# Kernel tuning notes

Hardware: AMD Instinct MI355X
Metric: run time of the kernel (lower is better)

The kernel has to match this reference:

```python
import jax, jax.numpy as jnp
import numpy as np

T = 100.0  # temperature, from init_kwargs
B = 4096
D = 128
NUM_CLASSES = 10


def setup_inputs() -> dict:
    key = jax.random.key(0)
    kx, ky = jax.random.split(key)
    x = jax.random.normal(kx, (B, D), dtype=jnp.float32)
    y = jax.random.randint(ky, (B,), 0, NUM_CLASSES, dtype=jnp.int64)
    return {"x": x, "y": y}


def reference(x, y):
    # Pairwise squared Euclidean distances: dist[i,j] = ||x_i - x_j||^2
    sq = jnp.sum(x * x, axis=1)                      # [b]
    dist = sq[:, None] + sq[None, :] - 2.0 * (x @ x.T)  # [b, b]
    dist = jnp.maximum(dist, 0.0)                    # clamp fp error; diag -> 0

    e = jnp.exp(-dist / T)                           # [b, b]; e[i,i] = 1

    b = x.shape[0]
    same = (y[:, None] == y[None, :])                # same-label mask
    not_self = ~jnp.eye(b, dtype=bool)

    # numerator: sum over j != i with y[j] == y[i]
    num = jnp.sum(jnp.where(same & not_self, e, 0.0), axis=1)  # [b]
    # denominator: sum over ALL j, including j == i (exp(0) = 1), as in the
    # original loop where the denominator accumulates unconditionally
    den = jnp.sum(e, axis=1)                         # [b]

    return jnp.mean(-jnp.log(num / den))
```

## Files before the change

kernel.cpp:

```cpp
#include <hip/hip_runtime.h>
#include <hip/hip_bf16.h>

#define NB 4096
#define DD 128

typedef short v8s __attribute__((ext_vector_type(8)));
typedef float v4f __attribute__((ext_vector_type(4)));


__global__ __launch_bounds__(256) void prep_kernel(const float* __restrict__ x,
        float* __restrict__ sq, float* __restrict__ num, float* __restrict__ den,
        float* __restrict__ out, unsigned short* __restrict__ xb) {
    int tid = threadIdx.x;
    int row = blockIdx.x * 8 + (tid >> 5);
    int lane = tid & 31;
    const float4* xg = (const float4*)x;
    float4 v = xg[row * 32 + lane];
    __hip_bfloat16 h0 = __float2bfloat16(v.x), h1 = __float2bfloat16(v.y);
    __hip_bfloat16 h2 = __float2bfloat16(v.z), h3 = __float2bfloat16(v.w);
    ushort4 u4;
    u4.x = *(unsigned short*)&h0; u4.y = *(unsigned short*)&h1;
    u4.z = *(unsigned short*)&h2; u4.w = *(unsigned short*)&h3;
    ((ushort4*)xb)[row * 32 + lane] = u4;
    float s = v.x * v.x + v.y * v.y + v.z * v.z + v.w * v.w;
    #pragma unroll
    for (int off = 16; off > 0; off >>= 1) s += __shfl_down(s, off);
    if (lane == 0) sq[row] = s;
    int gid = blockIdx.x * 256 + tid;
    if (gid < NB) { num[gid] = 0.f; den[gid] = 0.f; }
    if (gid == 0) out[0] = 0.f;
}

__global__ __launch_bounds__(256) void snn_mfma(const unsigned short* __restrict__ xb,
        const int* __restrict__ y, const float* __restrict__ sqg,
        float* __restrict__ num, float* __restrict__ den) {
    __shared__ __align__(16) union {
        unsigned short tiles[2 * 128 * 136];
        float part[2 * 128 * 34];
    } sm;
    __shared__ float sqi[128], sqj[128];
    __shared__ int yi[128], yj[128];

    const int tid = threadIdx.x;
    const int wave = tid >> 6;
    const int lane = tid & 63;
    const int wm = wave >> 1;
    const int wn = wave & 1;
    const int lr = lane & 15;
    const int q  = lane >> 4;
    const int i0 = blockIdx.x * 128;
    const int j0 = blockIdx.y * 128;

    const v8s* xg = (const v8s*)xb;
    unsigned short* At = sm.tiles;
    unsigned short* Bt = sm.tiles + 128 * 136;

    #pragma unroll
    for (int r = 0; r < 8; ++r) {
        int c = r * 256 + tid;
        int row = c >> 4, cc = c & 15;
        *(v8s*)&At[row * 136 + cc * 8] = xg[(i0 + row) * 16 + cc];
        *(v8s*)&Bt[row * 136 + cc * 8] = xg[(j0 + row) * 16 + cc];
    }
    if (tid < 128) {
        sqi[tid] = sqg[i0 + tid]; sqj[tid] = sqg[j0 + tid];
        yi[tid] = y[i0 + tid];    yj[tid] = y[j0 + tid];
    }
    __syncthreads();

    v4f acc[4][4];
    #pragma unroll
    for (int mt = 0; mt < 4; ++mt)
        #pragma unroll
        for (int nt = 0; nt < 4; ++nt)
            #pragma unroll
            for (int r = 0; r < 4; ++r) acc[mt][nt][r] = 0.f;

    #pragma unroll
    for (int kk = 0; kk < 4; ++kk) {
        v8s af[4], bf[4];
        #pragma unroll
        for (int mt = 0; mt < 4; ++mt)
            af[mt] = *(const v8s*)&At[(wm * 64 + mt * 16 + lr) * 136 + kk * 32 + q * 8];
        #pragma unroll
        for (int nt = 0; nt < 4; ++nt)
            bf[nt] = *(const v8s*)&Bt[(wn * 64 + nt * 16 + lr) * 136 + kk * 32 + q * 8];
        #pragma unroll
        for (int mt = 0; mt < 4; ++mt)
            #pragma unroll
            for (int nt = 0; nt < 4; ++nt)
                acc[mt][nt] = __builtin_amdgcn_mfma_f32_16x16x32_bf16(
                    af[mt], bf[nt], acc[mt][nt], 0, 0, 0);
    }

    __syncthreads();

    float sqj_r[4]; int yj_r[4], jg[4];
    #pragma unroll
    for (int nt = 0; nt < 4; ++nt) {
        int jc = wn * 64 + nt * 16 + lr;
        sqj_r[nt] = sqj[jc]; yj_r[nt] = yj[jc]; jg[nt] = j0 + jc;
    }
    #pragma unroll
    for (int mt = 0; mt < 4; ++mt) {
        #pragma unroll
        for (int r = 0; r < 4; ++r) {
            int rloc = wm * 64 + mt * 16 + q * 4 + r;
            float si = sqi[rloc]; int yir = yi[rloc]; int ig = i0 + rloc;
            float n = 0.f, d = 0.f;
            #pragma unroll
            for (int nt = 0; nt < 4; ++nt) {
                float dist = fmaxf(si + sqj_r[nt] - 2.f * acc[mt][nt][r], 0.f);
                float e = __builtin_amdgcn_exp2f(dist * -0.014426950408889634f);
                d += e;
                bool ok = (yir == yj_r[nt]) && (ig != jg[nt]);
                n += ok ? e : 0.f;
            }
            *(float2*)&sm.part[((wn * 128 + rloc) * 17 + lr) * 2] = make_float2(n, d);
        }
    }
    __syncthreads();

    {
        int row = tid >> 1, h = tid & 1;
        const float2* p = (const float2*)&sm.part[(h * 128 + row) * 34];
        float sn = 0.f, sd = 0.f;
        #pragma unroll
        for (int c = 0; c < 16; ++c) { float2 v = p[c]; sn += v.x; sd += v.y; }
        sn += __shfl_down(sn, 1); sd += __shfl_down(sd, 1);
        if (h == 0) {
            atomicAdd(&num[i0 + row], sn);
            atomicAdd(&den[i0 + row], sd);
        }
    }
}

__global__ __launch_bounds__(256) void snn_final(const float* __restrict__ num,
        const float* __restrict__ den, float* __restrict__ out) {
    __shared__ float wsum[4];
    int i = blockIdx.x * 256 + threadIdx.x;
    float l = -__logf(num[i] / den[i]);
    #pragma unroll
    for (int off = 32; off > 0; off >>= 1) l += __shfl_down(l, off);
    int wid = threadIdx.x >> 6;
    if ((threadIdx.x & 63) == 0) wsum[wid] = l;
    __syncthreads();
    if (threadIdx.x == 0) {
        float s = wsum[0] + wsum[1] + wsum[2] + wsum[3];
        atomicAdd(out, s * (1.0f / NB));
    }
}

extern "C" void kernel_launch(void* const* d_in, const int* in_sizes, int n_in,
                              void* d_out, int out_size, void* d_ws, size_t ws_size,
                              hipStream_t stream) {
    const float* x = (const float*)d_in[0];
    const int*   y = (const int*)d_in[1];
    float* out = (float*)d_out;
    float* sq  = (float*)d_ws;
    float* num = sq + NB;
    float* den = num + NB;
    unsigned short* xb = (unsigned short*)(den + NB);

    prep_kernel<<<NB / 8, 256, 0, stream>>>(x, sq, num, den, out, xb);
    dim3 grid(NB / 128, NB / 128);
    snn_mfma<<<grid, 256, 0, stream>>>(xb, y, sq, num, den);
    snn_final<<<NB / 256, 256, 0, stream>>>(num, den, out);
}
```

Measured before the change: 71.20 us.

## Fuse bf16 conversion and norms into MFMA kernel; replace atomics with partials

Removes the separate prep kernel. The main MFMA kernel now loads fp32 x directly, converts each tile to bf16 in shared memory and computes the row squared norms from those bf16 tiles. Per-row num/den atomics are replaced by a per-column-block partials buffer, which the final kernel sums before taking logs. This saves a launch, the zeroing pass and atomic contention. In exchange each block reads twice as many bytes (fp32 instead of bf16) with redundant conversion work, and the norms are now computed from bf16-rounded values.

```diff
diff --git a/kernel.cpp b/kernel.cpp
--- a/kernel.cpp
+++ b/kernel.cpp
@@ -2,38 +2,18 @@
 #include <hip/hip_bf16.h>
 
 #define NB 4096
-#define DD 128
 
 typedef short v8s __attribute__((ext_vector_type(8)));
 typedef float v4f __attribute__((ext_vector_type(4)));
 
-
-__global__ __launch_bounds__(256) void prep_kernel(const float* __restrict__ x,
-        float* __restrict__ sq, float* __restrict__ num, float* __restrict__ den,
-        float* __restrict__ out, unsigned short* __restrict__ xb) {
-    int tid = threadIdx.x;
-    int row = blockIdx.x * 8 + (tid >> 5);
-    int lane = tid & 31;
-    const float4* xg = (const float4*)x;
-    float4 v = xg[row * 32 + lane];
-    __hip_bfloat16 h0 = __float2bfloat16(v.x), h1 = __float2bfloat16(v.y);
-    __hip_bfloat16 h2 = __float2bfloat16(v.z), h3 = __float2bfloat16(v.w);
-    ushort4 u4;
-    u4.x = *(unsigned short*)&h0; u4.y = *(unsigned short*)&h1;
-    u4.z = *(unsigned short*)&h2; u4.w = *(unsigned short*)&h3;
-    ((ushort4*)xb)[row * 32 + lane] = u4;
-    float s = v.x * v.x + v.y * v.y + v.z * v.z + v.w * v.w;
-    #pragma unroll
-    for (int off = 16; off > 0; off >>= 1) s += __shfl_down(s, off);
-    if (lane == 0) sq[row] = s;
-    int gid = blockIdx.x * 256 + tid;
-    if (gid < NB) { num[gid] = 0.f; den[gid] = 0.f; }
-    if (gid == 0) out[0] = 0.f;
+__device__ __forceinline__ float bf2f(unsigned short u) {
+    return __uint_as_float(((unsigned int)u) << 16);
 }
 
-__global__ __launch_bounds__(256) void snn_mfma(const unsigned short* __restrict__ xb,
-        const int* __restrict__ y, const float* __restrict__ sqg,
-        float* __restrict__ num, float* __restrict__ den) {
+
+__global__ __launch_bounds__(256) void snn_mfma(const float* __restrict__ x,
+        const int* __restrict__ y, float2* __restrict__ part,
+        float* __restrict__ out) {
     __shared__ __align__(16) union {
         unsigned short tiles[2 * 128 * 136];
         float part[2 * 128 * 34];
@@ -51,22 +31,52 @@
     const int i0 = blockIdx.x * 128;
     const int j0 = blockIdx.y * 128;
 
-    const v8s* xg = (const v8s*)xb;
+    if (blockIdx.x == 0 && blockIdx.y == 0 && tid == 0) out[0] = 0.f;
+
     unsigned short* At = sm.tiles;
     unsigned short* Bt = sm.tiles + 128 * 136;
+    const float4* xg = (const float4*)x;
 
     #pragma unroll
-    for (int r = 0; r < 8; ++r) {
-        int c = r * 256 + tid;
-        int row = c >> 4, cc = c & 15;
-        *(v8s*)&At[row * 136 + cc * 8] = xg[(i0 + row) * 16 + cc];
-        *(v8s*)&Bt[row * 136 + cc * 8] = xg[(j0 + row) * 16 + cc];
+    for (int it = 0; it < 8; ++it) {
+        int p = it * 256 + tid;
+        int row = p >> 4, c2 = p & 15;
+        float4 a0 = xg[(i0 + row) * 32 + c2 * 2];
+        float4 a1 = xg[(i0 + row) * 32 + c2 * 2 + 1];
+        float4 b0 = xg[(j0 + row) * 32 + c2 * 2];
+        float4 b1 = xg[(j0 + row) * 32 + c2 * 2 + 1];
+        v8s av, bv;
+        const float af_[8] = {a0.x, a0.y, a0.z, a0.w, a1.x, a1.y, a1.z, a1.w};
+        const float bf_[8] = {b0.x, b0.y, b0.z, b0.w, b1.x, b1.y, b1.z, b1.w};
+        #pragma unroll
+        for (int e = 0; e < 8; ++e) {
+            __hip_bfloat16 ha = __float2bfloat16(af_[e]);
+            __hip_bfloat16 hb = __float2bfloat16(bf_[e]);
+            av[e] = *(short*)&ha;
+            bv[e] = *(short*)&hb;
+        }
+        *(v8s*)&At[row * 136 + c2 * 8] = av;
+        *(v8s*)&Bt[row * 136 + c2 * 8] = bv;
     }
-    if (tid < 128) {
-        sqi[tid] = sqg[i0 + tid]; sqj[tid] = sqg[j0 + tid];
-        yi[tid] = y[i0 + tid];    yj[tid] = y[j0 + tid];
+    if (tid < 128) yi[tid] = y[i0 + tid];
+    else           yj[tid - 128] = y[j0 + tid - 128];
+    __syncthreads();
+
+    {
+        int r = tid & 127;
+        const v8s* rp = (const v8s*)((tid < 128) ? &At[r * 136] : &Bt[r * 136]);
+        float s = 0.f;
+        #pragma unroll
+        for (int c = 0; c < 16; ++c) {
+            v8s v = rp[c];
+            #pragma unroll
+            for (int e = 0; e < 8; ++e) {
+                float f = bf2f((unsigned short)v[e]);
+                s += f * f;
+            }
+        }
+        if (tid < 128) sqi[r] = s; else sqj[r] = s;
     }
-    __syncthreads();
 
     v4f acc[4][4];
     #pragma unroll
@@ -128,18 +138,22 @@
         #pragma unroll
         for (int c = 0; c < 16; ++c) { float2 v = p[c]; sn += v.x; sd += v.y; }
         sn += __shfl_down(sn, 1); sd += __shfl_down(sd, 1);
-        if (h == 0) {
-            atomicAdd(&num[i0 + row], sn);
-            atomicAdd(&den[i0 + row], sd);
-        }
+        if (h == 0) part[(i0 + row) * 32 + blockIdx.y] = make_float2(sn, sd);
     }
 }
 
-__global__ __launch_bounds__(256) void snn_final(const float* __restrict__ num,
-        const float* __restrict__ den, float* __restrict__ out) {
+__global__ __launch_bounds__(256) void snn_final(const float2* __restrict__ part,
+        float* __restrict__ out) {
     __shared__ float wsum[4];
-    int i = blockIdx.x * 256 + threadIdx.x;
-    float l = -__logf(num[i] / den[i]);
+    int row = blockIdx.x * 256 + threadIdx.x;
+    const float4* p = (const float4*)&part[row * 32];
+    float n = 0.f, d = 0.f;
+    #pragma unroll
+    for (int c = 0; c < 16; ++c) {
+        float4 v = p[c];
+        n += v.x + v.z; d += v.y + v.w;
+    }
+    float l = __logf(d) - __logf(n);
     #pragma unroll
     for (int off = 32; off > 0; off >>= 1) l += __shfl_down(l, off);
     int wid = threadIdx.x >> 6;
@@ -157,13 +171,9 @@
     const float* x = (const float*)d_in[0];
     const int*   y = (const int*)d_in[1];
     float* out = (float*)d_out;
-    float* sq  = (float*)d_ws;
-    float* num = sq + NB;
-    float* den = num + NB;
-    unsigned short* xb = (unsigned short*)(den + NB);
+    float2* part = (float2*)d_ws;
 
-    prep_kernel<<<NB / 8, 256, 0, stream>>>(x, sq, num, den, out, xb);
     dim3 grid(NB / 128, NB / 128);
-    snn_mfma<<<grid, 256, 0, stream>>>(xb, y, sq, num, den);
-    snn_final<<<NB / 256, 256, 0, stream>>>(num, den, out);
+    snn_mfma<<<grid, 256, 0, stream>>>(x, y, part, out);
+    snn_final<<<NB / 256, 256, 0, stream>>>(part, out);
 }
```

New measurement: 73.32 us. 1.03x slower.

## Exploit distance symmetry with triangular tile grid and deterministic partial sums

Applied to the files above, without the earlier changes.

Launches only the upper-triangular 128x128 tile blocks (528 instead of 1024). Each off-diagonal tile adds its row and column partial sums, so the symmetric half of the distance matrix is never computed. Global atomics are replaced by a per-row, per-tile-column partial buffer that the final kernel reduces, which also removes the zero-initialisation of num and den. Squared norms are now computed from bf16-rounded values so they match the MFMA dot products. The cost is extra column reductions, a larger workspace buffer, and a sqrt-based tile index decode.

```diff
diff --git a/kernel.cpp b/kernel.cpp
--- a/kernel.cpp
+++ b/kernel.cpp
@@ -2,15 +2,14 @@
 #include <hip/hip_bf16.h>
 
 #define NB 4096
-#define DD 128
 
 typedef short v8s __attribute__((ext_vector_type(8)));
 typedef float v4f __attribute__((ext_vector_type(4)));
 
 
 __global__ __launch_bounds__(256) void prep_kernel(const float* __restrict__ x,
-        float* __restrict__ sq, float* __restrict__ num, float* __restrict__ den,
-        float* __restrict__ out, unsigned short* __restrict__ xb) {
+        float* __restrict__ sq, unsigned short* __restrict__ xb,
+        float* __restrict__ out) {
     int tid = threadIdx.x;
     int row = blockIdx.x * 8 + (tid >> 5);
     int lane = tid & 31;
@@ -22,24 +21,25 @@
     u4.x = *(unsigned short*)&h0; u4.y = *(unsigned short*)&h1;
     u4.z = *(unsigned short*)&h2; u4.w = *(unsigned short*)&h3;
     ((ushort4*)xb)[row * 32 + lane] = u4;
-    float s = v.x * v.x + v.y * v.y + v.z * v.z + v.w * v.w;
+    float f0 = __bfloat162float(h0), f1 = __bfloat162float(h1);
+    float f2 = __bfloat162float(h2), f3 = __bfloat162float(h3);
+    float s = f0 * f0 + f1 * f1 + f2 * f2 + f3 * f3;
     #pragma unroll
     for (int off = 16; off > 0; off >>= 1) s += __shfl_down(s, off);
     if (lane == 0) sq[row] = s;
-    int gid = blockIdx.x * 256 + tid;
-    if (gid < NB) { num[gid] = 0.f; den[gid] = 0.f; }
-    if (gid == 0) out[0] = 0.f;
+    if (blockIdx.x == 0 && tid == 0) out[0] = 0.f;
 }
 
 __global__ __launch_bounds__(256) void snn_mfma(const unsigned short* __restrict__ xb,
         const int* __restrict__ y, const float* __restrict__ sqg,
-        float* __restrict__ num, float* __restrict__ den) {
+        float2* __restrict__ part) {
     __shared__ __align__(16) union {
         unsigned short tiles[2 * 128 * 136];
         float part[2 * 128 * 34];
     } sm;
     __shared__ float sqi[128], sqj[128];
     __shared__ int yi[128], yj[128];
+    float2* partC = (float2*)&sm.part[2 * 128 * 34];
 
     const int tid = threadIdx.x;
     const int wave = tid >> 6;
@@ -48,12 +48,19 @@
     const int wn = wave & 1;
     const int lr = lane & 15;
     const int q  = lane >> 4;
-    const int i0 = blockIdx.x * 128;
-    const int j0 = blockIdx.y * 128;
 
-    const v8s* xg = (const v8s*)xb;
+    int t = blockIdx.x;
+    int by = (int)((sqrtf(8.0f * (float)t + 1.0f) - 1.0f) * 0.5f);
+    if (by * (by + 1) / 2 > t) --by;
+    if ((by + 1) * (by + 2) / 2 <= t) ++by;
+    int bx = t - by * (by + 1) / 2;
+    const int i0 = bx * 128;
+    const int j0 = by * 128;
+    const bool offdiag = (bx != by);
+
     unsigned short* At = sm.tiles;
     unsigned short* Bt = sm.tiles + 128 * 136;
+    const v8s* xg = (const v8s*)xb;
 
     #pragma unroll
     for (int r = 0; r < 8; ++r) {
@@ -62,10 +69,8 @@
         *(v8s*)&At[row * 136 + cc * 8] = xg[(i0 + row) * 16 + cc];
         *(v8s*)&Bt[row * 136 + cc * 8] = xg[(j0 + row) * 16 + cc];
     }
-    if (tid < 128) {
-        sqi[tid] = sqg[i0 + tid]; sqj[tid] = sqg[j0 + tid];
-        yi[tid] = y[i0 + tid];    yj[tid] = y[j0 + tid];
-    }
+    if (tid < 128) { sqi[tid] = sqg[i0 + tid]; yi[tid] = y[i0 + tid]; }
+    else { sqj[tid - 128] = sqg[j0 + tid - 128]; yj[tid - 128] = y[j0 + tid - 128]; }
     __syncthreads();
 
     v4f acc[4][4];
@@ -101,6 +106,9 @@
         int jc = wn * 64 + nt * 16 + lr;
         sqj_r[nt] = sqj[jc]; yj_r[nt] = yj[jc]; jg[nt] = j0 + jc;
     }
+    float colN[4] = {0.f, 0.f, 0.f, 0.f};
+    float colD[4] = {0.f, 0.f, 0.f, 0.f};
+
     #pragma unroll
     for (int mt = 0; mt < 4; ++mt) {
         #pragma unroll
@@ -114,9 +122,21 @@
                 float e = __builtin_amdgcn_exp2f(dist * -0.014426950408889634f);
                 d += e;
                 bool ok = (yir == yj_r[nt]) && (ig != jg[nt]);
-                n += ok ? e : 0.f;
+                float ne = ok ? e : 0.f;
+                n += ne;
+                colN[nt] += ne;
+                colD[nt] += e;
             }
             *(float2*)&sm.part[((wn * 128 + rloc) * 17 + lr) * 2] = make_float2(n, d);
+        }
+    }
+    if (offdiag) {
+        #pragma unroll
+        for (int nt = 0; nt < 4; ++nt) {
+            float cn = colN[nt], cd = colD[nt];
+            cn += __shfl_xor(cn, 16); cd += __shfl_xor(cd, 16);
+            cn += __shfl_xor(cn, 32); cd += __shfl_xor(cd, 32);
+            if (q == 0) partC[wm * 128 + wn * 64 + nt * 16 + lr] = make_float2(cn, cd);
         }
     }
     __syncthreads();
@@ -128,18 +148,26 @@
         #pragma unroll
         for (int c = 0; c < 16; ++c) { float2 v = p[c]; sn += v.x; sd += v.y; }
         sn += __shfl_down(sn, 1); sd += __shfl_down(sd, 1);
-        if (h == 0) {
-            atomicAdd(&num[i0 + row], sn);
-            atomicAdd(&den[i0 + row], sd);
-        }
+        if (h == 0) part[(i0 + row) * 32 + by] = make_float2(sn, sd);
+    }
+    if (offdiag && tid < 128) {
+        float2 a = partC[tid], b = partC[128 + tid];
+        part[(j0 + tid) * 32 + bx] = make_float2(a.x + b.x, a.y + b.y);
     }
 }
 
-__global__ __launch_bounds__(256) void snn_final(const float* __restrict__ num,
-        const float* __restrict__ den, float* __restrict__ out) {
+__global__ __launch_bounds__(256) void snn_final(const float2* __restrict__ part,
+        float* __restrict__ out) {
     __shared__ float wsum[4];
-    int i = blockIdx.x * 256 + threadIdx.x;
-    float l = -__logf(num[i] / den[i]);
+    int row = blockIdx.x * 256 + threadIdx.x;
+    const float4* p = (const float4*)&part[row * 32];
+    float n = 0.f, d = 0.f;
+    #pragma unroll
+    for (int c = 0; c < 16; ++c) {
+        float4 v = p[c];
+        n += v.x + v.z; d += v.y + v.w;
+    }
+    float l = __logf(d) - __logf(n);
     #pragma unroll
     for (int off = 32; off > 0; off >>= 1) l += __shfl_down(l, off);
     int wid = threadIdx.x >> 6;
@@ -157,13 +185,11 @@
     const float* x = (const float*)d_in[0];
     const int*   y = (const int*)d_in[1];
     float* out = (float*)d_out;
-    float* sq  = (float*)d_ws;
-    float* num = sq + NB;
-    float* den = num + NB;
-    unsigned short* xb = (unsigned short*)(den + NB);
+    float2* part = (float2*)d_ws;
+    float* sq = (float*)((char*)d_ws + (1 << 20));
+    unsigned short* xb = (unsigned short*)((char*)d_ws + (1 << 20) + (16 << 10));
 
-    prep_kernel<<<NB / 8, 256, 0, stream>>>(x, sq, num, den, out, xb);
-    dim3 grid(NB / 128, NB / 128);
-    snn_mfma<<<grid, 256, 0, stream>>>(xb, y, sq, num, den);
-    snn_final<<<NB / 256, 256, 0, stream>>>(num, den, out);
+    prep_kernel<<<NB / 8, 256, 0, stream>>>(x, sq, xb, out);
+    snn_mfma<<<528, 256, 0, stream>>>(xb, y, sq, part);
+    snn_final<<<NB / 256, 256, 0, stream>>>(part, out);
 }
```

Measured after the change: 72.34 us. About the same (+1.6%).
